# Optimization experiments

Hardware: AMD Instinct MI355X
Metric: run time of the kernel (lower is better)

The kernel has to match this reference:

```python
import jax, jax.numpy as jnp
import numpy as np
from jax import lax

B, C, H, W = 32, 512, 32, 32
NH = 8
ER = 4
DK_RATIO = 0.2
EPS_LN = 1e-6


def _layernorm(t, g, b):
    m = t.mean(-1, keepdims=True)
    v = ((t - m) ** 2).mean(-1, keepdims=True)
    return (t - m) / jnp.sqrt(v + EPS_LN) * g + b


def setup_inputs() -> dict:
    key = jax.random.key(0)
    ks = jax.random.split(key, 24)
    s = 0.02
    dh = C // NH
    return {
        "x": jax.random.normal(ks[0], (B, C, H, W), jnp.float32),
        "mask_u": jax.random.uniform(ks[1], (B, NH, dh, dh), jnp.float32),
        "dw_w": jax.random.normal(ks[2], (C, 1, 3, 3), jnp.float32) * s,
        "dw_b": jnp.zeros((C,), jnp.float32),
        "ln1_g": jnp.ones((C,), jnp.float32),
        "ln1_b": jnp.zeros((C,), jnp.float32),
        "qkv_w": jax.random.normal(ks[3], (3 * C, C), jnp.float32) * s,
        "qkv_b": jnp.zeros((3 * C,), jnp.float32),
        "temp": jnp.ones((NH, 1, 1), jnp.float32),
        "proj_w": jax.random.normal(ks[4], (C, C), jnp.float32) * s,
        "proj_b": jnp.zeros((C,), jnp.float32),
        "ct_w": jax.random.normal(ks[5], (C, C, 2, 2), jnp.float32) * s,  # [in,out,kH,kW]
        "ct_b": jnp.zeros((C,), jnp.float32),
        "ln2_g": jnp.ones((C,), jnp.float32),
        "ln2_b": jnp.zeros((C,), jnp.float32),
        "pw1_w": jax.random.normal(ks[6], (ER * C, C), jnp.float32) * s,
        "pw1_b": jnp.zeros((ER * C,), jnp.float32),
        "pw2_w": jax.random.normal(ks[7], (C, ER * C), jnp.float32) * s,
        "pw2_b": jnp.zeros((C,), jnp.float32),
    }


def reference(x, mask_u, dw_w, dw_b, ln1_g, ln1_b, qkv_w, qkv_b, temp,
              proj_w, proj_b, ct_w, ct_b, ln2_g, ln2_b,
              pw1_w, pw1_b, pw2_w, pw2_b):
    inp = x
    b, c, h, w = x.shape
    # depthwise 3x3 conv + residual
    dw = lax.conv_general_dilated(
        x, dw_w, (1, 1), "SAME", feature_group_count=c,
        dimension_numbers=("NCHW", "OIHW", "NCHW")) + dw_b[None, :, None, None]
    x = dw + inp
    # 2x2 avg pool, stride 2
    hp, wp = h // 2, w // 2
    x = x.reshape(b, c, hp, 2, wp, 2).mean(axis=(3, 5))  # [B,C,hp,wp]
    n = hp * wp
    # tokens [B,N,C] -> LN -> qkv
    t = x.reshape(b, c, n).transpose(0, 2, 1)
    t = _layernorm(t, ln1_g, ln1_b)
    qkv = t @ qkv_w.T + qkv_b                       # [B,N,3C]
    dh = c // NH
    qkv = qkv.reshape(b, n, 3, NH, dh).transpose(2, 0, 3, 1, 4)  # [3,B,h,N,d]
    # cosine (XCA-style) attention: transpose to [B,h,d,N], normalize over N
    q = jnp.swapaxes(qkv[0], -2, -1)
    k = jnp.swapaxes(qkv[1], -2, -1)
    v = jnp.swapaxes(qkv[2], -2, -1)
    q = q / jnp.maximum(jnp.linalg.norm(q, axis=-1, keepdims=True), 1e-12)
    k = k / jnp.maximum(jnp.linalg.norm(k, axis=-1, keepdims=True), 1e-12)
    attn = jnp.einsum("bhdn,bhen->bhde", q, k) * temp  # [B,h,d,d]
    attn = attn + (mask_u < DK_RATIO).astype(attn.dtype) * (-1e12)
    attn = jax.nn.softmax(attn, axis=-1)
    out = jnp.einsum("bhde,bhen->bhdn", attn, v)       # [B,h,d,N]
    out = out.transpose(0, 3, 1, 2).reshape(b, n, c)
    t = out @ proj_w.T + proj_b
    t = t + t
    x = t.transpose(0, 2, 1).reshape(b, c, hp, wp)
    # ConvTranspose2d(C,C,2,stride=2): each pixel expands to 2x2 block
    x = jnp.einsum("bchw,copq->bohpwq", x, ct_w).reshape(b, c, 2 * hp, 2 * wp)
    x = x + ct_b[None, :, None, None]
    # MLP in channels-last
    y = x.transpose(0, 2, 3, 1)                        # [B,H,W,C]
    y = _layernorm(y, ln2_g, ln2_b)
    y = jax.nn.gelu(y @ pw1_w.T + pw1_b, approximate=False)
    y = y @ pw2_w.T + pw2_b
    x = y.transpose(0, 3, 1, 2)
    return inp + x
```

## Files before the change

kernel.cpp:

```cpp
#include <hip/hip_runtime.h>
#include <hip/hip_bf16.h>
#include <math.h>

typedef unsigned short ushort;
typedef __attribute__((ext_vector_type(8))) short short8;
typedef __attribute__((ext_vector_type(8))) unsigned short ushort8;
typedef __attribute__((ext_vector_type(4))) unsigned short ushort4v;
typedef __attribute__((ext_vector_type(4))) float f32x4;

__device__ __forceinline__ ushort f2bb(float v) {
    return __builtin_bit_cast(ushort, __float2bfloat16(v));
}
__device__ __forceinline__ float bf2f(ushort u) {
    return __bfloat162float(__builtin_bit_cast(__hip_bfloat16, u));
}
__device__ __forceinline__ void gl2lds16(const ushort* g, ushort* l) {
    __builtin_amdgcn_global_load_lds(
        (const __attribute__((address_space(1))) unsigned int*)g,
        (__attribute__((address_space(3))) unsigned int*)l, 16, 0, 0);
}


__global__ __launch_bounds__(256) void cvtw_k(const float* __restrict__ in,
                                              ushort* __restrict__ out, int n4) {
    int i = blockIdx.x * 256 + threadIdx.x;
    if (i >= n4) return;
    float4 v = ((const float4*)in)[i];
    ushort4v o;
    o.x = f2bb(v.x); o.y = f2bb(v.y); o.z = f2bb(v.z); o.w = f2bb(v.w);
    ((ushort4v*)out)[i] = o;
}

__global__ __launch_bounds__(256) void cvtt_k(const float* __restrict__ in,
                                              ushort* __restrict__ out) {
    __shared__ float tl[32][33];
    int c0 = blockIdx.y * 32, j0 = blockIdx.x * 32;
    int tr = threadIdx.x >> 5, tc = threadIdx.x & 31;
#pragma unroll
    for (int p4 = 0; p4 < 4; ++p4)
        tl[tr + p4 * 8][tc] = in[(size_t)(c0 + tr + p4 * 8) * 2048 + j0 + tc];
    __syncthreads();
#pragma unroll
    for (int p4 = 0; p4 < 4; ++p4)
        out[(size_t)(j0 + tr + p4 * 8) * 512 + c0 + tc] = f2bb(tl[tc][tr + p4 * 8]);
}

__global__ __launch_bounds__(256) void dwpool_k(const float* __restrict__ x,
                                                const float* __restrict__ dww,
                                                const float* __restrict__ dwb,
                                                ushort* __restrict__ xp) {
    int bc = blockIdx.x;
    int c = bc & 511;
    __shared__ float tile[32][33];
    __shared__ float w9[9];
    const float* xb = x + (size_t)bc * 1024;
    int tid = threadIdx.x;
    for (int i = tid; i < 1024; i += 256) tile[i >> 5][i & 31] = xb[i];
    if (tid < 9) w9[tid] = dww[c * 9 + tid];
    __syncthreads();
    float bv = dwb[c];
    int ph = tid >> 4, pw = tid & 15;
    float s = 0.f;
#pragma unroll
    for (int dy = 0; dy < 2; ++dy) {
#pragma unroll
        for (int dx = 0; dx < 2; ++dx) {
            int hh = 2 * ph + dy, ww = 2 * pw + dx;
            float a = bv + tile[hh][ww];
#pragma unroll
            for (int ky = 0; ky < 3; ++ky) {
                int yy = hh + ky - 1;
                if (yy < 0 || yy > 31) continue;
#pragma unroll
                for (int kx = 0; kx < 3; ++kx) {
                    int xx = ww + kx - 1;
                    if (xx < 0 || xx > 31) continue;
                    a += w9[ky * 3 + kx] * tile[yy][xx];
                }
            }
            s += a;
        }
    }
    xp[(size_t)bc * 256 + tid] = f2bb(0.25f * s);
}

__global__ __launch_bounds__(256) void ln1_stats_k(const ushort* __restrict__ xp,
                                                   float* __restrict__ m1,
                                                   float* __restrict__ r1) {
    __shared__ float sh_s[4][64], sh_q[4][64];
    int blk = blockIdx.x;
    int b = blk >> 2;
    int n0 = (blk & 3) * 64;
    int t = threadIdx.x & 63, w = threadIdx.x >> 6;
    float s = 0.f, ss = 0.f;
    for (int i = 0; i < 128; ++i) {
        int c = w * 128 + i;
        float v = bf2f(xp[(size_t)(b * 512 + c) * 256 + n0 + t]);
        s += v; ss += v * v;
    }
    sh_s[w][t] = s; sh_q[w][t] = ss;
    __syncthreads();
    if (w == 0) {
        s  = sh_s[0][t] + sh_s[1][t] + sh_s[2][t] + sh_s[3][t];
        ss = sh_q[0][t] + sh_q[1][t] + sh_q[2][t] + sh_q[3][t];
        float m = s * (1.0f / 512.0f);
        m1[b * 256 + n0 + t] = m;
        r1[b * 256 + n0 + t] = rsqrtf(ss * (1.0f / 512.0f) - m * m + 1e-6f);
    }
}

__global__ __launch_bounds__(256) void ln1_apply_k(const ushort* __restrict__ xp,
                                                   const float* __restrict__ m1,
                                                   const float* __restrict__ r1,
                                                   const float* __restrict__ g,
                                                   const float* __restrict__ beta,
                                                   ushort* __restrict__ a_ln) {
    __shared__ float tl[64][66];
    int blk = blockIdx.x;
    int b = blk >> 5, ct = (blk >> 2) & 7, nt = blk & 3;
    int t = threadIdx.x;
    int rq = t >> 6, nl = t & 63;
#pragma unroll
    for (int i = 0; i < 16; ++i) {
        int r = rq * 16 + i;
        int c = ct * 64 + r;
        tl[r][nl] = bf2f(xp[(size_t)(b * 512 + c) * 256 + nt * 64 + nl]);
    }
    __syncthreads();
    int r2 = t >> 2, cq = t & 3;
    int m = b * 256 + nt * 64 + r2;
    float mu = m1[m], rs = r1[m];
#pragma unroll
    for (int hh = 0; hh < 2; ++hh) {
        ushort8 o;
#pragma unroll
        for (int j = 0; j < 8; ++j) {
            int cl = cq * 16 + hh * 8 + j;
            int c = ct * 64 + cl;
            o[j] = f2bb((tl[cl][r2] - mu) * rs * g[c] + beta[c]);
        }
        *(ushort8*)&a_ln[(size_t)m * 512 + ct * 64 + cq * 16 + hh * 8] = o;
    }
}

__global__ __launch_bounds__(256) void ln2_fuse_k(ushort* __restrict__ yB,
                                                  ushort* __restrict__ yT,
                                                  const float* __restrict__ g,
                                                  const float* __restrict__ beta) {
    int w = threadIdx.x >> 6, lane = threadIdx.x & 63;
    int row = blockIdx.x * 4 + w;
    ushort* base = (row < 8192) ? (yB + (size_t)row * 512)
                                : (yT + (size_t)(row - 8192) * 512);
    ushort8 raw = *(ushort8*)&base[lane * 8];
    float v[8];
    float s = 0.f, ss = 0.f;
#pragma unroll
    for (int j = 0; j < 8; ++j) { v[j] = bf2f(raw[j]); s += v[j]; ss += v[j] * v[j]; }
#pragma unroll
    for (int off = 1; off < 64; off <<= 1) { s += __shfl_xor(s, off); ss += __shfl_xor(ss, off); }
    float mu = s * (1.0f / 512.0f);
    float rs = rsqrtf(ss * (1.0f / 512.0f) - mu * mu + 1e-6f);
    ushort8 o;
#pragma unroll
    for (int j = 0; j < 8; ++j) {
        int c = lane * 8 + j;
        o[j] = f2bb((v[j] - mu) * rs * g[c] + beta[c]);
    }
    *(ushort8*)&base[lane * 8] = o;
}

struct GP {
    const ushort* A;
    const ushort* W;
    const float* bias;
    ushort* outB;
    ushort* outB2;
    float* outF;
    const float* inp;
    int K, m0;
};

template <int MODE, int BN>
__global__ __launch_bounds__(256) void mgemm_k(GP p) {
    constexpr int MT = (BN == 128) ? 4 : 2;
    constexpr int NT = 4;
    constexpr int SMEM_BYTES = (MODE == 2) ? 20480 : ((MODE == 4) ? 16896 : 16384);
    __shared__ __align__(16) char smem[SMEM_BYTES];
    ushort* As = (ushort*)smem;
    ushort* Bs = As + 128 * 32;
    int tid = threadIdx.x;
    int lane = tid & 63, w = tid >> 6;
    int lr = lane & 15, lq = lane >> 4;
    int mwoff = (BN == 128) ? (w >> 1) * 64 : w * 32;
    int nwoff = (BN == 128) ? (w & 1) * 64 : 0;
    int gx = gridDim.x;
    int wgid = blockIdx.y * gx + blockIdx.x;
    int cpx = (gx * gridDim.y) >> 3;
    int swz = (wgid & 7) * cpx + (wgid >> 3);
    int bx = swz % gx, by = swz / gx;
    int mbase = by * 128, nbase = bx * BN;
    int lsub = lane >> 2;
    int cchunk = (lane & 3) ^ ((lsub >> 1) & 3);
    int lcol = cchunk * 8;
    int physc = lq ^ ((lr >> 1) & 3);
    f32x4 acc[MT][NT] = {};

    for (int kb = 0; kb < p.K; kb += 32) {
        __syncthreads();
#pragma unroll
        for (int i = 0; i < 2; ++i) {
            int row = w * 32 + i * 16;
            gl2lds16(p.A + (size_t)(mbase + row + lsub) * p.K + kb + lcol,
                     &As[row * 32]);
        }
        if constexpr (BN == 128) {
#pragma unroll
            for (int i = 0; i < 2; ++i) {
                int row = w * 32 + i * 16;
                gl2lds16(p.W + (size_t)(nbase + row + lsub) * p.K + kb + lcol,
                         &Bs[row * 32]);
            }
        } else {
            int row = w * 16;
            gl2lds16(p.W + (size_t)(nbase + row + lsub) * p.K + kb + lcol,
                     &Bs[row * 32]);
        }
        __syncthreads();
        short8 af[MT], bfr[NT];
#pragma unroll
        for (int t = 0; t < MT; ++t)
            af[t] = *(const short8*)&As[(mwoff + t * 16 + lr) * 32 + physc * 8];
#pragma unroll
        for (int t = 0; t < NT; ++t)
            bfr[t] = *(const short8*)&Bs[(nwoff + t * 16 + lr) * 32 + physc * 8];
#pragma unroll
        for (int i = 0; i < MT; ++i)
#pragma unroll
            for (int j = 0; j < NT; ++j)
                acc[i][j] = __builtin_amdgcn_mfma_f32_16x16x32_bf16(af[i], bfr[j], acc[i][j], 0, 0, 0);
    }

    if constexpr (MODE == 1 || MODE == 3) {
        const size_t LD = (MODE == 1) ? 512 : 2048;
        ushort* eb = (ushort*)smem;
#pragma unroll
        for (int h = 0; h < 2; ++h) {
            __syncthreads();
            if ((w & 1) == h) {
#pragma unroll
                for (int ti = 0; ti < MT; ++ti)
#pragma unroll
                    for (int tj = 0; tj < NT; ++tj)
#pragma unroll
                        for (int r = 0; r < 4; ++r) {
                            int row = mwoff + ti * 16 + lq * 4 + r;
                            int colh = tj * 16 + lr;
                            float v = acc[ti][tj][r] + p.bias[nbase + h * 64 + colh];
                            if constexpr (MODE == 1) v *= 2.0f;
                            else v = 0.5f * v * (1.0f + erff(v * 0.70710678118654752f));
                            int ph = (colh >> 3) ^ (row & 7);
                            eb[row * 64 + ph * 8 + (colh & 7)] = f2bb(v);
                        }
            }
            __syncthreads();
#pragma unroll
            for (int i = 0; i < 4; ++i) {
                int row = i * 32 + (tid >> 3);
                int ch = tid & 7;
                int pch = ch ^ (row & 7);
                short8 d = *(short8*)&eb[row * 64 + pch * 8];
                *(short8*)&p.outB[(size_t)(mbase + row) * LD + nbase + h * 64 + ch * 8] = d;
            }
        }
    } else if constexpr (MODE == 0) {
        ushort* eb = (ushort*)smem;
        int b = mbase >> 8, n0 = mbase & 255;
#pragma unroll
        for (int pc = 0; pc < 4; ++pc) {
            __syncthreads();
            if ((w & 1) == (pc >> 1)) {
                int tjb = (pc & 1) * 2;
#pragma unroll
                for (int ti = 0; ti < MT; ++ti)
#pragma unroll
                    for (int tj2 = 0; tj2 < 2; ++tj2)
#pragma unroll
                        for (int r = 0; r < 4; ++r) {
                            int tj = tjb + tj2;
                            int row = mwoff + ti * 16 + lq * 4 + r;
                            int cl = tj2 * 16 + lr;
                            float v = acc[ti][tj][r] + p.bias[nbase + pc * 32 + cl];
                            eb[cl * 136 + row] = f2bb(v);
                        }
            }
            __syncthreads();
#pragma unroll
            for (int i = 0; i < 2; ++i) {
                int dl = (tid >> 4) + 16 * i;
                int ch = tid & 15;
                short8 d = *(short8*)&eb[dl * 136 + ch * 8];
                int cg = nbase + pc * 32 + dl;
                int sect = cg >> 9, hh = (cg >> 6) & 7, dd = cg & 63;
                size_t addr = ((size_t)(sect * 256 + b * 8 + hh) * 64 + dd) * 256 + n0 + ch * 8;
                *(short8*)&p.outB[addr] = d;
            }
        }
    } else if constexpr (MODE == 2) {
        ushort* eb = (ushort*)smem;
        ushort* ybase = (mbase < 2048) ? p.outB : (p.outB2 - (size_t)8192 * 512);
        int obase = nbase >> 2;
#pragma unroll
        for (int hf = 0; hf < 2; ++hf) {
            __syncthreads();
            if ((w >> 1) == hf) {
#pragma unroll
                for (int ti = 0; ti < MT; ++ti)
#pragma unroll
                    for (int tj = 0; tj < NT; ++tj)
#pragma unroll
                        for (int r = 0; r < 4; ++r) {
                            int rl = (mwoff - hf * 64) + ti * 16 + lq * 4 + r;
                            int cgl = nwoff + tj * 16 + lr;
                            int o_l = cgl >> 2, pp = (cgl >> 1) & 1, qq = cgl & 1;
                            int pix = ((rl >> 4) * 2 + pp) * 32 + (rl & 15) * 2 + qq;
                            float v = acc[ti][tj][r] + p.bias[obase + o_l];
                            eb[pix * 40 + o_l] = f2bb(v);
                        }
            }
            __syncthreads();
            int hhbase = ((mbase & 255) >> 4) + hf * 4;
            int prb = (mbase >> 8) * 32 + 2 * hhbase;
#pragma unroll
            for (int i = 0; i < 4; ++i) {
                int pix = i * 64 + (tid >> 2);
                int ch = tid & 3;
                short8 d = *(short8*)&eb[pix * 40 + ch * 8];
                int pr = (prb + (pix >> 5)) * 32 + (pix & 31);
                *(short8*)&ybase[(size_t)pr * 512 + obase + ch * 8] = d;
            }
        }
    } else {
        float* ef = (float*)smem;
        int gm0 = p.m0 + mbase;
        int b = gm0 >> 10, hw0 = gm0 & 1023;
#pragma unroll
        for (int pc = 0; pc < 2; ++pc) {
            __syncthreads();
#pragma unroll
            for (int ti = 0; ti < MT; ++ti)
#pragma unroll
                for (int tj2 = 0; tj2 < 2; ++tj2)
#pragma unroll
                    for (int r = 0; r < 4; ++r) {
                        int tj = pc * 2 + tj2;
                        int row = mwoff + ti * 16 + lq * 4 + r;
                        int cl = tj2 * 16 + lr;
                        ef[cl * 132 + row] = acc[ti][tj][r] + p.bias[nbase + pc * 32 + cl];
                    }
            __syncthreads();
#pragma unroll
            for (int i = 0; i < 4; ++i) {
                int cl = (tid >> 5) + 8 * i;
                int ck = tid & 31;
                float4 v4 = *(float4*)&ef[cl * 132 + ck * 4];
                int c = nbase + pc * 32 + cl;
                size_t idx = ((size_t)(b * 512 + c)) * 1024 + hw0 + ck * 4;
                float4 xin = *(const float4*)&p.inp[idx];
                float4 o4;
                o4.x = xin.x + v4.x; o4.y = xin.y + v4.y;
                o4.z = xin.z + v4.z; o4.w = xin.w + v4.w;
                *(float4*)&p.outF[idx] = o4;
            }
        }
    }
}

__global__ __launch_bounds__(256) void attn_k(const ushort* __restrict__ qkvp,
                                              const float* __restrict__ mask_u,
                                              const float* __restrict__ temp,
                                              ushort* __restrict__ attn_out) {
    __shared__ float bufA[64 * 65];
    __shared__ float bufB[64 * 65];
    __shared__ float Sb[64 * 65];
    __shared__ float fq[64], fk[64];
    int tid = threadIdx.x;
    int bh = blockIdx.x;
    int b = bh >> 3, h = bh & 7;
    const ushort* q = qkvp + (size_t)bh * 16384;
    const ushort* k = qkvp + 4194304 + (size_t)bh * 16384;
    const ushort* v = qkvp + 8388608 + (size_t)bh * 16384;
    int wv = tid >> 6, lane = tid & 63;

    for (int rr = 0; rr < 16; ++rr) {
        int row = wv * 16 + rr;
        float s = 0.f;
#pragma unroll
        for (int i = 0; i < 4; ++i) { float xv = bf2f(q[row * 256 + lane + i * 64]); s += xv * xv; }
#pragma unroll
        for (int off = 32; off; off >>= 1) s += __shfl_down(s, off);
        if (lane == 0) fq[row] = 1.0f / fmaxf(sqrtf(s), 1e-12f);
        s = 0.f;
#pragma unroll
        for (int i = 0; i < 4; ++i) { float xv = bf2f(k[row * 256 + lane + i * 64]); s += xv * xv; }
#pragma unroll
        for (int off = 32; off; off >>= 1) s += __shfl_down(s, off);
        if (lane == 0) fk[row] = 1.0f / fmaxf(sqrtf(s), 1e-12f);
    }
    __syncthreads();

    int tx = tid & 15, ty = tid >> 4;
    float acc[4][4] = {};
    for (int nb = 0; nb < 256; nb += 64) {
        __syncthreads();
#pragma unroll
        for (int it = 0; it < 16; ++it) {
            int f = it * 256 + tid;
            int d = f >> 6, n = f & 63;
            bufA[d * 65 + n] = bf2f(q[d * 256 + nb + n]);
            bufB[d * 65 + n] = bf2f(k[d * 256 + nb + n]);
        }
        __syncthreads();
#pragma unroll 8
        for (int kk = 0; kk < 64; ++kk) {
            float a[4], bb[4];
#pragma unroll
            for (int i = 0; i < 4; ++i) a[i] = bufA[(ty * 4 + i) * 65 + kk];
#pragma unroll
            for (int j = 0; j < 4; ++j) bb[j] = bufB[(tx * 4 + j) * 65 + kk];
#pragma unroll
            for (int i = 0; i < 4; ++i)
#pragma unroll
                for (int j = 0; j < 4; ++j) acc[i][j] += a[i] * bb[j];
        }
    }
    float tv = temp[h];
    __syncthreads();
#pragma unroll
    for (int i = 0; i < 4; ++i) {
        int d = ty * 4 + i;
#pragma unroll
        for (int j = 0; j < 4; ++j) {
            int e = tx * 4 + j;
            float sc = acc[i][j] * fq[d] * fk[e] * tv;
            float mu = mask_u[((size_t)bh * 64 + d) * 64 + e];
            if (mu < 0.2f) sc -= 1e12f;
            Sb[d * 65 + e] = sc;
        }
    }
    __syncthreads();

    {
        int row = tid >> 2, sub = tid & 3;
        float ev[16];
        float mx = -INFINITY;
#pragma unroll
        for (int i = 0; i < 16; ++i) { float s = Sb[row * 65 + sub * 16 + i]; ev[i] = s; mx = fmaxf(mx, s); }
        mx = fmaxf(mx, __shfl_xor(mx, 1));
        mx = fmaxf(mx, __shfl_xor(mx, 2));
        float sum = 0.f;
#pragma unroll
        for (int i = 0; i < 16; ++i) { ev[i] = expf(ev[i] - mx); sum += ev[i]; }
        sum += __shfl_xor(sum, 1);
        sum += __shfl_xor(sum, 2);
        float inv = 1.0f / sum;
#pragma unroll
        for (int i = 0; i < 16; ++i) Sb[row * 65 + sub * 16 + i] = ev[i] * inv;
    }
    __syncthreads();

    for (int nb = 0; nb < 256; nb += 64) {
        __syncthreads();
#pragma unroll
        for (int it = 0; it < 16; ++it) {
            int f = it * 256 + tid;
            int e = f >> 6, n = f & 63;
            bufA[e * 65 + n] = bf2f(v[e * 256 + nb + n]);
        }
        __syncthreads();
        float o[4][4] = {};
#pragma unroll 8
        for (int kk = 0; kk < 64; ++kk) {
            float a[4], bb[4];
#pragma unroll
            for (int i = 0; i < 4; ++i) a[i] = Sb[(ty * 4 + i) * 65 + kk];
#pragma unroll
            for (int j = 0; j < 4; ++j) bb[j] = bufA[kk * 65 + tx * 4 + j];
#pragma unroll
            for (int i = 0; i < 4; ++i)
#pragma unroll
                for (int j = 0; j < 4; ++j) o[i][j] += a[i] * bb[j];
        }
#pragma unroll
        for (int j = 0; j < 4; ++j) {
            int n = nb + tx * 4 + j;
            size_t base = ((size_t)(b * 256 + n)) * 512 + h * 64 + ty * 4;
#pragma unroll
            for (int i = 0; i < 4; ++i) attn_out[base + i] = f2bb(o[i][j]);
        }
    }
}

extern "C" void kernel_launch(void* const* d_in, const int* in_sizes, int n_in,
                              void* d_out, int out_size, void* d_ws, size_t ws_size,
                              hipStream_t stream) {
    const float* x      = (const float*)d_in[0];
    const float* mask_u = (const float*)d_in[1];
    const float* dw_w   = (const float*)d_in[2];
    const float* dw_b   = (const float*)d_in[3];
    const float* ln1_g  = (const float*)d_in[4];
    const float* ln1_b  = (const float*)d_in[5];
    const float* qkv_w  = (const float*)d_in[6];
    const float* qkv_b  = (const float*)d_in[7];
    const float* temp   = (const float*)d_in[8];
    const float* proj_w = (const float*)d_in[9];
    const float* proj_b = (const float*)d_in[10];
    const float* ct_w   = (const float*)d_in[11];
    const float* ct_b   = (const float*)d_in[12];
    const float* ln2_g  = (const float*)d_in[13];
    const float* ln2_b  = (const float*)d_in[14];
    const float* pw1_w  = (const float*)d_in[15];
    const float* pw1_b  = (const float*)d_in[16];
    const float* pw2_w  = (const float*)d_in[17];
    const float* pw2_b  = (const float*)d_in[18];

    char* wsb = (char*)d_ws;
    float* mean1 = (float*)wsb;
    float* rstd1 = mean1 + 8192;
    ushort* wq = (ushort*)(wsb + 524288);
    ushort* wp = wq + 786432;
    ushort* wc = wp + 262144;
    ushort* w1 = wc + 1048576;
    ushort* w2 = w1 + 1048576;
    ushort* xp     = (ushort*)(wsb + 8912896);
    ushort* t2     = xp;
    ushort* a_ln   = (ushort*)(wsb + 17301504);
    ushort* yB     = a_ln;
    ushort* qkvp   = (ushort*)(wsb + 25690112);
    ushort* attn_o = (ushort*)(wsb + 50855936);
    ushort* h1c    = qkvp;
    ushort* yT     = (ushort*)(wsb + 59244544);

    cvtw_k<<<768,  256, 0, stream>>>(qkv_w,  wq, 196608);
    cvtw_k<<<256,  256, 0, stream>>>(proj_w, wp, 65536);
    cvtw_k<<<1024, 256, 0, stream>>>(pw1_w,  w1, 262144);
    cvtw_k<<<1024, 256, 0, stream>>>(pw2_w,  w2, 262144);
    cvtt_k<<<dim3(64, 16), 256, 0, stream>>>(ct_w, wc);
    dwpool_k<<<32 * 512, 256, 0, stream>>>(x, dw_w, dw_b, xp);
    ln1_stats_k<<<128, 256, 0, stream>>>(xp, mean1, rstd1);
    ln1_apply_k<<<1024, 256, 0, stream>>>(xp, mean1, rstd1, ln1_g, ln1_b, a_ln);
    {
        GP p{}; p.A = a_ln; p.W = wq; p.bias = qkv_b; p.outB = qkvp; p.K = 512;
        mgemm_k<0, 128><<<dim3(12, 64), 256, 0, stream>>>(p);
    }
    attn_k<<<256, 256, 0, stream>>>(qkvp, mask_u, temp, attn_o);
    {
        GP p{}; p.A = attn_o; p.W = wp; p.bias = proj_b; p.outB = t2; p.K = 512;
        mgemm_k<1, 128><<<dim3(4, 64), 256, 0, stream>>>(p);
    }
    {
        GP p{}; p.A = t2; p.W = wc; p.bias = ct_b;
        p.outB = yB; p.outB2 = yT; p.K = 512;
        mgemm_k<2, 128><<<dim3(16, 64), 256, 0, stream>>>(p);
    }
    ln2_fuse_k<<<8192, 256, 0, stream>>>(yB, yT, ln2_g, ln2_b);
    for (int c = 0; c < 4; ++c) {
        int m0 = c * 8192;
        const ushort* yChunk = (c == 0) ? yB : (yT + (size_t)(m0 - 8192) * 512);
        {
            GP p{}; p.A = yChunk; p.W = w1; p.bias = pw1_b; p.outB = h1c; p.K = 512;
            mgemm_k<3, 128><<<dim3(16, 64), 256, 0, stream>>>(p);
        }
        {
            GP p{}; p.A = h1c; p.W = w2; p.bias = pw2_b;
            p.outF = (float*)d_out; p.inp = x; p.K = 2048; p.m0 = m0;
            mgemm_k<4, 64><<<dim3(8, 64), 256, 0, stream>>>(p);
        }
    }
}
```

Baseline: 714.9 us.

## Double-buffer LDS tiles in the MFMA GEMM main loop

The bf16 MFMA GEMM kernel now keeps two LDS buffers for the A and B tiles. It issues the async global-to-LDS load for the next K-block before computing on the current one, which also cuts the loop to one barrier per iteration instead of two. The intent is to hide global load latency behind the MFMA work. In exchange the kernel uses roughly twice as much LDS, which may lower how many workgroups fit on each compute unit.

Result: faster. 671.5 us (-6.1%).

```diff
diff --git a/kernel.cpp b/kernel.cpp
--- a/kernel.cpp
+++ b/kernel.cpp
@@ -184,10 +184,10 @@
 __global__ __launch_bounds__(256) void mgemm_k(GP p) {
     constexpr int MT = (BN == 128) ? 4 : 2;
     constexpr int NT = 4;
-    constexpr int SMEM_BYTES = (MODE == 2) ? 20480 : ((MODE == 4) ? 16896 : 16384);
-    __shared__ __align__(16) char smem[SMEM_BYTES];
-    ushort* As = (ushort*)smem;
-    ushort* Bs = As + 128 * 32;
+    constexpr int ATILE = 128 * 32;
+    constexpr int BTILE = BN * 32;
+    constexpr int SMEM_US = 2 * (ATILE + BTILE);
+    __shared__ __align__(16) ushort smem[SMEM_US];
     int tid = threadIdx.x;
     int lane = tid & 63, w = tid >> 6;
     int lr = lane & 15, lq = lane >> 4;
@@ -205,39 +205,50 @@
     int physc = lq ^ ((lr >> 1) & 3);
     f32x4 acc[MT][NT] = {};
 
-    for (int kb = 0; kb < p.K; kb += 32) {
-        __syncthreads();
+    auto stage = [&](int buf, int kb) {
+        ushort* Ab = smem + buf * ATILE;
+        ushort* Bb = smem + 2 * ATILE + buf * BTILE;
 #pragma unroll
         for (int i = 0; i < 2; ++i) {
             int row = w * 32 + i * 16;
             gl2lds16(p.A + (size_t)(mbase + row + lsub) * p.K + kb + lcol,
-                     &As[row * 32]);
+                     &Ab[row * 32]);
         }
         if constexpr (BN == 128) {
 #pragma unroll
             for (int i = 0; i < 2; ++i) {
                 int row = w * 32 + i * 16;
                 gl2lds16(p.W + (size_t)(nbase + row + lsub) * p.K + kb + lcol,
-                         &Bs[row * 32]);
+                         &Bb[row * 32]);
             }
         } else {
             int row = w * 16;
             gl2lds16(p.W + (size_t)(nbase + row + lsub) * p.K + kb + lcol,
-                     &Bs[row * 32]);
-        }
-        __syncthreads();
+                     &Bb[row * 32]);
+        }
+    };
+
+    stage(0, 0);
+    __syncthreads();
+    int nk = p.K >> 5;
+    for (int t = 0; t < nk; ++t) {
+        int cur = t & 1;
+        if (t + 1 < nk) stage(cur ^ 1, (t + 1) << 5);
+        const ushort* Ac = smem + cur * ATILE;
+        const ushort* Bc = smem + 2 * ATILE + cur * BTILE;
         short8 af[MT], bfr[NT];
 #pragma unroll
-        for (int t = 0; t < MT; ++t)
-            af[t] = *(const short8*)&As[(mwoff + t * 16 + lr) * 32 + physc * 8];
-#pragma unroll
-        for (int t = 0; t < NT; ++t)
-            bfr[t] = *(const short8*)&Bs[(nwoff + t * 16 + lr) * 32 + physc * 8];
+        for (int tt = 0; tt < MT; ++tt)
+            af[tt] = *(const short8*)&Ac[(mwoff + tt * 16 + lr) * 32 + physc * 8];
+#pragma unroll
+        for (int tt = 0; tt < NT; ++tt)
+            bfr[tt] = *(const short8*)&Bc[(nwoff + tt * 16 + lr) * 32 + physc * 8];
 #pragma unroll
         for (int i = 0; i < MT; ++i)
 #pragma unroll
             for (int j = 0; j < NT; ++j)
                 acc[i][j] = __builtin_amdgcn_mfma_f32_16x16x32_bf16(af[i], bfr[j], acc[i][j], 0, 0, 0);
+        __syncthreads();
     }
 
     if constexpr (MODE == 1 || MODE == 3) {
```
